# Performance work log

Hardware: AMD Instinct MI355X
Metric: run time of the kernel (lower is better)

Reference implementation:

```python
import jax, jax.numpy as jnp
import numpy as np

B, S, D_MODEL, H, D_K, D_V = 2, 2048, 1024, 16, 64, 64


def setup_inputs() -> dict:
    key = jax.random.key(0)
    ks = jax.random.split(key, 12)
    s = 0.02
    inp = {
        "Q": jax.random.normal(ks[0], (B, S, D_MODEL), jnp.float32),
        "K": jax.random.normal(ks[1], (B, S, D_MODEL), jnp.float32),
        "V": jax.random.normal(ks[2], (B, S, D_MODEL), jnp.float32),
        # causal 0/1 mask, broadcastable to [B, H, S, S]
        "mask": jnp.tril(jnp.ones((S, S), jnp.int32))[None, None, :, :],
        "Wq": jax.random.normal(ks[3], (D_MODEL, H * D_K), jnp.float32) * s,
        "bq": jnp.zeros((H * D_K,), jnp.float32),
        "Wk": jax.random.normal(ks[4], (D_MODEL, H * D_K), jnp.float32) * s,
        "bk": jnp.zeros((H * D_K,), jnp.float32),
        "Wv": jax.random.normal(ks[5], (D_MODEL, H * D_V), jnp.float32) * s,
        "bv": jnp.zeros((H * D_V,), jnp.float32),
        "Wo": jax.random.normal(ks[6], (H * D_V, D_MODEL), jnp.float32) * s,
        "bo": jnp.zeros((D_MODEL,), jnp.float32),
    }
    return inp


def reference(Q, K, V, mask, Wq, bq, Wk, bk, Wv, bv, Wo, bo):
    b = Q.shape[0]
    # project and split heads: [B, S, H*dk] -> [B, H, S, dk]
    q = (Q @ Wq + bq).reshape(b, -1, H, D_K).transpose(0, 2, 1, 3)
    k = (K @ Wk + bk).reshape(b, -1, H, D_K).transpose(0, 2, 1, 3)
    v = (V @ Wv + bv).reshape(b, -1, H, D_V).transpose(0, 2, 1, 3)
    scale = 1.0 / np.sqrt(D_K).astype(np.float32)
    scores = jnp.einsum("bhqd,bhkd->bhqk", q, k) * scale
    scores = jnp.where(mask == 0, jnp.float32(-1e9), scores)
    attn = jax.nn.softmax(scores, axis=-1)
    context = jnp.einsum("bhqk,bhkd->bhqd", attn, v)
    context = context.transpose(0, 2, 1, 3).reshape(b, -1, H * D_V)
    output = context @ Wo + bo  # dropout is identity in eval
    return output, attn
```

## Files before the change

### kernel.cpp

```cpp
#include <hip/hip_runtime.h>
#include <math.h>

#define S_LEN 2048
#define DMODEL 1024
#define NHEAD 16
#define HD 64
#define NBATCH 2

using short8  = __attribute__((ext_vector_type(8))) short;
using ushort8 = __attribute__((ext_vector_type(8))) unsigned short;
using floatx4 = __attribute__((ext_vector_type(4))) float;

__device__ __forceinline__ unsigned short f2b(float f) {
    unsigned int u = __float_as_uint(f);
    unsigned int r = (u + 0x7FFFu + ((u >> 16) & 1u)) >> 16;
    return (unsigned short)r;
}
__device__ __forceinline__ float b2f(unsigned short b) {
    return __uint_as_float(((unsigned int)b) << 16);
}

__device__ __forceinline__ void gll16(const void* g, void* l) {
    __builtin_amdgcn_global_load_lds(
        (const __attribute__((address_space(1))) unsigned int*)g,
        (__attribute__((address_space(3))) unsigned int*)l, 16, 0, 0);
}

__global__ __launch_bounds__(256)
void convert_bf16(const float* __restrict__ S0, const float* __restrict__ S1,
                  const float* __restrict__ S2,
                  unsigned short* __restrict__ D0, unsigned short* __restrict__ D1,
                  unsigned short* __restrict__ D2, int n4)
{
    const float* src = (blockIdx.z == 0) ? S0 : (blockIdx.z == 1) ? S1 : S2;
    unsigned short* dst = (blockIdx.z == 0) ? D0 : (blockIdx.z == 1) ? D1 : D2;
    int i = blockIdx.x * 256 + threadIdx.x;
    if (i < n4) {
        float4 v = ((const float4*)src)[i];
        ushort4 o;
        o.x = f2b(v.x); o.y = f2b(v.y); o.z = f2b(v.z); o.w = f2b(v.w);
        ((ushort4*)dst)[i] = o;
    }
}

__global__ __launch_bounds__(256)
void transpose_w(const float* __restrict__ W0, const float* __restrict__ W1,
                 const float* __restrict__ W2, const float* __restrict__ W3,
                 unsigned short* __restrict__ T0, unsigned short* __restrict__ T1,
                 unsigned short* __restrict__ T2, unsigned short* __restrict__ T3)
{
    __shared__ float t[64][65];
    const float* W; unsigned short* T;
    switch (blockIdx.z) {
        case 0: W = W0; T = T0; break;
        case 1: W = W1; T = T1; break;
        case 2: W = W2; T = T2; break;
        default: W = W3; T = T3; break;
    }
    const int tid = threadIdx.x;
    const int c0 = blockIdx.x * 64;
    const int r0 = blockIdx.y * 64;
    #pragma unroll
    for (int i = 0; i < 4; ++i) {
        int c = tid + i * 256;
        int r = c >> 4, off = (c & 15) * 4;
        float4 v = *(const float4*)(W + (size_t)(r0 + r) * DMODEL + c0 + off);
        t[r][off + 0] = v.x; t[r][off + 1] = v.y;
        t[r][off + 2] = v.z; t[r][off + 3] = v.w;
    }
    __syncthreads();
    #pragma unroll
    for (int i = 0; i < 4; ++i) {
        int c = tid + i * 256;
        int n = c >> 4, off = (c & 15) * 4;
        ushort4 o;
        o.x = f2b(t[off + 0][n]); o.y = f2b(t[off + 1][n]);
        o.z = f2b(t[off + 2][n]); o.w = f2b(t[off + 3][n]);
        *(ushort4*)(T + (size_t)(c0 + n) * DMODEL + r0 + off) = o;
    }
}

__global__ __launch_bounds__(256)
void gemm_qkv(const unsigned short* __restrict__ X0, const unsigned short* __restrict__ X1,
              const unsigned short* __restrict__ X2,
              const unsigned short* __restrict__ W0, const unsigned short* __restrict__ W1,
              const unsigned short* __restrict__ W2,
              const float* __restrict__ b0, const float* __restrict__ b1,
              const float* __restrict__ b2,
              unsigned short* __restrict__ o0, unsigned short* __restrict__ o1,
              unsigned short* __restrict__ o2)
{
    __shared__ unsigned short Xs[128 * 64];
    __shared__ unsigned short Ws[128 * 64];

    const unsigned short* X  = (blockIdx.z == 0) ? X0 : (blockIdx.z == 1) ? X1 : X2;
    const unsigned short* Wt = (blockIdx.z == 0) ? W0 : (blockIdx.z == 1) ? W1 : W2;
    const float* bias        = (blockIdx.z == 0) ? b0 : (blockIdx.z == 1) ? b1 : b2;
    unsigned short* outp     = (blockIdx.z == 0) ? o0 : (blockIdx.z == 1) ? o1 : o2;

    const int tid = threadIdx.x;
    const int lane = tid & 63, w = tid >> 6;
    const int l15 = lane & 15, l4 = lane >> 4;
    const int wr = w >> 1, wc = w & 1;
    const int row0 = blockIdx.y * 128;
    const int col0 = blockIdx.x * 128;

    const int srow = lane >> 3;
    const int sblk = (lane & 7) ^ srow;

    floatx4 acc[4][4] = {};

    for (int k0 = 0; k0 < DMODEL; k0 += 64) {
        __syncthreads();
        #pragma unroll
        for (int i = 0; i < 4; ++i)
            gll16(X + (size_t)(row0 + w * 32 + i * 8 + srow) * DMODEL + k0 + sblk * 8,
                  &Xs[(w * 32 + i * 8) * 64]);
        #pragma unroll
        for (int i = 0; i < 4; ++i)
            gll16(Wt + (size_t)(col0 + w * 32 + i * 8 + srow) * DMODEL + k0 + sblk * 8,
                  &Ws[(w * 32 + i * 8) * 64]);
        asm volatile("s_waitcnt vmcnt(0)" ::: "memory");
        __syncthreads();

        #pragma unroll
        for (int ks = 0; ks < 2; ++ks) {
            short8 a[4], b[4];
            #pragma unroll
            for (int m = 0; m < 4; ++m) {
                const int r = wr * 64 + m * 16 + l15;
                a[m] = *(const short8*)&Xs[r * 64 + (((ks * 4 + l4) ^ (r & 7)) << 3)];
            }
            #pragma unroll
            for (int n = 0; n < 4; ++n) {
                const int r = wc * 64 + n * 16 + l15;
                b[n] = *(const short8*)&Ws[r * 64 + (((ks * 4 + l4) ^ (r & 7)) << 3)];
            }
            #pragma unroll
            for (int m = 0; m < 4; ++m)
                #pragma unroll
                for (int n = 0; n < 4; ++n)
                    acc[m][n] = __builtin_amdgcn_mfma_f32_16x16x32_bf16(
                        a[m], b[n], acc[m][n], 0, 0, 0);
        }
    }

    float bl[4];
    #pragma unroll
    for (int n = 0; n < 4; ++n)
        bl[n] = bias[col0 + wc * 64 + n * 16 + l15];

    if (blockIdx.z != 2) {
        #pragma unroll
        for (int m = 0; m < 4; ++m)
            #pragma unroll
            for (int n = 0; n < 4; ++n) {
                const int gc = col0 + wc * 64 + n * 16 + l15;
                const int h = gc >> 6, d = gc & 63;
                #pragma unroll
                for (int reg = 0; reg < 4; ++reg) {
                    const int gr = row0 + wr * 64 + m * 16 + l4 * 4 + reg;
                    const int bb = gr >> 11, s = gr & 2047;
                    outp[(((size_t)bb * NHEAD + h) * S_LEN + s) * HD + d] =
                        f2b(acc[m][n][reg] + bl[n]);
                }
            }
    } else {
        #pragma unroll
        for (int m = 0; m < 4; ++m)
            #pragma unroll
            for (int n = 0; n < 4; ++n) {
                const int gc = col0 + wc * 64 + n * 16 + l15;
                const int h = gc >> 6, d = gc & 63;
                const int s0 = row0 + wr * 64 + m * 16 + l4 * 4;
                const int bb = s0 >> 11, sr = s0 & 2047;
                ushort4 pk;
                pk.x = f2b(acc[m][n][0] + bl[n]);
                pk.y = f2b(acc[m][n][1] + bl[n]);
                pk.z = f2b(acc[m][n][2] + bl[n]);
                pk.w = f2b(acc[m][n][3] + bl[n]);
                *(ushort4*)(outp + (((size_t)bb * NHEAD + h) * HD + d) * S_LEN + sr) = pk;
            }
    }
}

__global__ __launch_bounds__(256)
void gemm_out(const unsigned short* __restrict__ X, const unsigned short* __restrict__ Wt,
              const float* __restrict__ bias, float* __restrict__ out)
{
    __shared__ unsigned short Xs[128 * 64];
    __shared__ unsigned short Ws[64 * 64];

    const int tid = threadIdx.x;
    const int lane = tid & 63, w = tid >> 6;
    const int l15 = lane & 15, l4 = lane >> 4;
    const int wr = w >> 1, wc = w & 1;
    const int row0 = blockIdx.y * 128;
    const int col0 = blockIdx.x * 64;

    const int srow = lane >> 3;
    const int sblk = (lane & 7) ^ srow;

    floatx4 acc[4][2] = {};

    for (int k0 = 0; k0 < DMODEL; k0 += 64) {
        __syncthreads();
        #pragma unroll
        for (int i = 0; i < 4; ++i)
            gll16(X + (size_t)(row0 + w * 32 + i * 8 + srow) * DMODEL + k0 + sblk * 8,
                  &Xs[(w * 32 + i * 8) * 64]);
        #pragma unroll
        for (int i = 0; i < 2; ++i)
            gll16(Wt + (size_t)(col0 + w * 16 + i * 8 + srow) * DMODEL + k0 + sblk * 8,
                  &Ws[(w * 16 + i * 8) * 64]);
        asm volatile("s_waitcnt vmcnt(0)" ::: "memory");
        __syncthreads();

        #pragma unroll
        for (int ks = 0; ks < 2; ++ks) {
            short8 a[4], b[2];
            #pragma unroll
            for (int m = 0; m < 4; ++m) {
                const int r = wr * 64 + m * 16 + l15;
                a[m] = *(const short8*)&Xs[r * 64 + (((ks * 4 + l4) ^ (r & 7)) << 3)];
            }
            #pragma unroll
            for (int n = 0; n < 2; ++n) {
                const int r = wc * 32 + n * 16 + l15;
                b[n] = *(const short8*)&Ws[r * 64 + (((ks * 4 + l4) ^ (r & 7)) << 3)];
            }
            #pragma unroll
            for (int m = 0; m < 4; ++m)
                #pragma unroll
                for (int n = 0; n < 2; ++n)
                    acc[m][n] = __builtin_amdgcn_mfma_f32_16x16x32_bf16(
                        a[m], b[n], acc[m][n], 0, 0, 0);
        }
    }

    float bl[2];
    #pragma unroll
    for (int n = 0; n < 2; ++n)
        bl[n] = bias[col0 + wc * 32 + n * 16 + l15];

    #pragma unroll
    for (int m = 0; m < 4; ++m)
        #pragma unroll
        for (int n = 0; n < 2; ++n) {
            const int gc = col0 + wc * 32 + n * 16 + l15;
            #pragma unroll
            for (int reg = 0; reg < 4; ++reg) {
                const int gr = row0 + wr * 64 + m * 16 + l4 * 4 + reg;
                out[(size_t)gr * DMODEL + gc] = acc[m][n][reg] + bl[n];
            }
        }
}

__global__ __launch_bounds__(256)
void attn_mfma(const unsigned short* __restrict__ qg, const unsigned short* __restrict__ kg,
               const unsigned short* __restrict__ vtg, float* __restrict__ attn,
               unsigned short* __restrict__ ctx)
{
    __shared__ unsigned short Ks[2 * 64 * 64];
    __shared__ unsigned short Vt[64 * 64];
    __shared__ unsigned short Ps[64 * 88];

    const int tid = threadIdx.x;
    const int lane = tid & 63, w = tid >> 6;
    const int l15 = lane & 15, l4 = lane >> 4;

    const int i0 = blockIdx.x;
    const int local = i0 >> 3;
    const int bh = (i0 & 7) * 4 + (local & 3);
    const int qx = local >> 2;
    const int qb = (bh & 1) ? (31 - qx) : qx;
    const int row0 = qb * 64;

    const int srow = lane >> 3;
    const int sblk = (lane & 7) ^ srow;

    const float C2 = 0.18033688011112042f;

    const unsigned short* qh = qg + (size_t)bh * S_LEN * HD;
    const unsigned short* kh = kg + (size_t)bh * S_LEN * HD;
    const unsigned short* vth = vtg + (size_t)bh * HD * S_LEN;
    float* attnh = attn + (size_t)bh * S_LEN * S_LEN;

    short8 qa[2];
    #pragma unroll
    for (int ks = 0; ks < 2; ++ks)
        qa[ks] = *(const short8*)(qh + (size_t)(row0 + w * 16 + l15) * HD + ks * 32 + l4 * 8);

    const int nt = qb + 1;

    #pragma unroll
    for (int i = 0; i < 2; ++i)
        gll16(kh + (size_t)(w * 16 + i * 8 + srow) * HD + sblk * 8,
              &Ks[(w * 16 + i * 8) * 64]);

    float lsum[4] = {};
    for (int jt = 0; jt < nt; ++jt) {
        const int cur = jt & 1;
        __syncthreads();
        if (jt + 1 < nt) {
            #pragma unroll
            for (int i = 0; i < 2; ++i)
                gll16(kh + (size_t)((jt + 1) * 64 + w * 16 + i * 8 + srow) * HD + sblk * 8,
                      &Ks[(cur ^ 1) * 4096 + (w * 16 + i * 8) * 64]);
            asm volatile("s_waitcnt vmcnt(2)" ::: "memory");
        } else {
            asm volatile("s_waitcnt vmcnt(0)" ::: "memory");
        }
        __syncthreads();

        floatx4 sf[4] = {};
        #pragma unroll
        for (int ks = 0; ks < 2; ++ks) {
            short8 kb[4];
            #pragma unroll
            for (int c = 0; c < 4; ++c) {
                const int r = c * 16 + l15;
                kb[c] = *(const short8*)&Ks[cur * 4096 + r * 64
                                            + (((ks * 4 + l4) ^ (r & 7)) << 3)];
            }
            #pragma unroll
            for (int c = 0; c < 4; ++c)
                sf[c] = __builtin_amdgcn_mfma_f32_16x16x32_bf16(qa[ks], kb[c], sf[c], 0, 0, 0);
        }

        const int rbase = row0 + w * 16;
        if (jt * 64 + 63 <= rbase) {
            #pragma unroll
            for (int c = 0; c < 4; ++c)
                #pragma unroll
                for (int reg = 0; reg < 4; ++reg)
                    lsum[reg] += exp2f(sf[c][reg] * C2);
        } else {
            #pragma unroll
            for (int c = 0; c < 4; ++c) {
                const int jcol = jt * 64 + c * 16 + l15;
                #pragma unroll
                for (int reg = 0; reg < 4; ++reg) {
                    const int grow = rbase + l4 * 4 + reg;
                    lsum[reg] += (jcol <= grow) ? exp2f(sf[c][reg] * C2) : 0.f;
                }
            }
        }
    }

    float nl2[4];
    #pragma unroll
    for (int reg = 0; reg < 4; ++reg) {
        float s = lsum[reg];
        #pragma unroll
        for (int off = 1; off < 16; off <<= 1)
            s += __shfl_xor(s, off);
        nl2[reg] = -__log2f(s);
    }

    floatx4 o[4] = {};

    __syncthreads();
    #pragma unroll
    for (int i = 0; i < 2; ++i)
        gll16(kh + (size_t)(w * 16 + i * 8 + srow) * HD + sblk * 8,
              &Ks[(w * 16 + i * 8) * 64]);

    for (int jt = 0; jt < nt; ++jt) {
        const int buf = jt & 1;
        asm volatile("s_waitcnt vmcnt(0)" ::: "memory");
        __syncthreads();

        #pragma unroll
        for (int i = 0; i < 2; ++i)
            gll16(vth + (size_t)(w * 16 + i * 8 + srow) * S_LEN + jt * 64 + sblk * 8,
                  &Vt[(w * 16 + i * 8) * 64]);
        if (jt + 1 < nt) {
            #pragma unroll
            for (int i = 0; i < 2; ++i)
                gll16(kh + (size_t)((jt + 1) * 64 + w * 16 + i * 8 + srow) * HD + sblk * 8,
                      &Ks[(buf ^ 1) * 4096 + (w * 16 + i * 8) * 64]);
        }

        floatx4 sf[4] = {};
        #pragma unroll
        for (int ks = 0; ks < 2; ++ks) {
            short8 kb[4];
            #pragma unroll
            for (int c = 0; c < 4; ++c) {
                const int r = c * 16 + l15;
                kb[c] = *(const short8*)&Ks[buf * 4096 + r * 64
                                            + (((ks * 4 + l4) ^ (r & 7)) << 3)];
            }
            #pragma unroll
            for (int c = 0; c < 4; ++c)
                sf[c] = __builtin_amdgcn_mfma_f32_16x16x32_bf16(qa[ks], kb[c], sf[c], 0, 0, 0);
        }

        const int rbase = row0 + w * 16;
        const bool full = (jt * 64 + 63 <= rbase);
        #pragma unroll
        for (int c = 0; c < 4; ++c) {
            const int jcol = jt * 64 + c * 16 + l15;
            #pragma unroll
            for (int reg = 0; reg < 4; ++reg) {
                const int rl = w * 16 + l4 * 4 + reg;
                float p = exp2f(fmaf(sf[c][reg], C2, nl2[reg]));
                if (!full && jcol > rbase + l4 * 4 + reg) p = 0.f;
                Ps[rl * 88 + c * 16 + l15] = f2b(p);
            }
        }
        if (jt + 1 < nt) {
            asm volatile("s_waitcnt vmcnt(2)" ::: "memory");
        } else {
            asm volatile("s_waitcnt vmcnt(0)" ::: "memory");
        }
        __syncthreads();

        #pragma unroll
        for (int i2 = 0; i2 < 4; ++i2) {
            const int idx = tid + i2 * 256;
            const int r = idx >> 4, c4 = (idx & 15) * 4;
            const ushort4 pb = *(const ushort4*)&Ps[r * 88 + c4];
            floatx4 pf;
            pf[0] = b2f(pb.x); pf[1] = b2f(pb.y); pf[2] = b2f(pb.z); pf[3] = b2f(pb.w);
            __builtin_nontemporal_store(
                pf, (floatx4*)(attnh + (size_t)(row0 + r) * S_LEN + jt * 64 + c4));
        }

        #pragma unroll
        for (int ks = 0; ks < 2; ++ks) {
            const short8 pa = *(const short8*)&Ps[(w * 16 + l15) * 88 + ks * 32 + l4 * 8];
            #pragma unroll
            for (int c = 0; c < 4; ++c) {
                const int r = c * 16 + l15;
                const short8 vb = *(const short8*)&Vt[r * 64
                                                     + (((ks * 4 + l4) ^ (r & 7)) << 3)];
                o[c] = __builtin_amdgcn_mfma_f32_16x16x32_bf16(pa, vb, o[c], 0, 0, 0);
            }
        }
    }

    const int b = bh >> 4, h = bh & 15;
    #pragma unroll
    for (int c = 0; c < 4; ++c)
        #pragma unroll
        for (int reg = 0; reg < 4; ++reg) {
            const int gr = row0 + w * 16 + l4 * 4 + reg;
            const int d = c * 16 + l15;
            ctx[((size_t)b * S_LEN + gr) * DMODEL + h * HD + d] = f2b(o[c][reg]);
        }

    const floatx4 z4 = {0.f, 0.f, 0.f, 0.f};
    for (int jt = nt; jt < S_LEN / 64; ++jt) {
        #pragma unroll
        for (int i = 0; i < 4; ++i) {
            const int idx = tid + i * 256;
            const int r = idx >> 4, off = (idx & 15) * 4;
            __builtin_nontemporal_store(
                z4, (floatx4*)(attnh + (size_t)(row0 + r) * S_LEN + jt * 64 + off));
        }
    }
}

extern "C" void kernel_launch(void* const* d_in, const int* in_sizes, int n_in,
                              void* d_out, int out_size, void* d_ws, size_t ws_size,
                              hipStream_t stream)
{
    const float* Q  = (const float*)d_in[0];
    const float* K  = (const float*)d_in[1];
    const float* V  = (const float*)d_in[2];
    const float* Wq = (const float*)d_in[4];
    const float* bq = (const float*)d_in[5];
    const float* Wk = (const float*)d_in[6];
    const float* bk = (const float*)d_in[7];
    const float* Wv = (const float*)d_in[8];
    const float* bv = (const float*)d_in[9];
    const float* Wo = (const float*)d_in[10];
    const float* bo = (const float*)d_in[11];

    float* out  = (float*)d_out;
    float* attn = out + (size_t)NBATCH * S_LEN * DMODEL;

    const size_t per = (size_t)NBATCH * S_LEN * DMODEL;
    const size_t wsz = (size_t)DMODEL * DMODEL;
    unsigned short* Xq  = (unsigned short*)d_ws;
    unsigned short* Xk  = Xq + per;
    unsigned short* Xv  = Xk + per;
    unsigned short* Wtq = Xv + per;
    unsigned short* Wtk = Wtq + wsz;
    unsigned short* Wtv = Wtk + wsz;
    unsigned short* Wto = Wtv + wsz;
    unsigned short* qhw = Wto + wsz;
    unsigned short* khw = qhw + per;
    unsigned short* vhw = khw + per;
    unsigned short* ctx = vhw + per;

    const int n4 = (int)(per / 4);
    convert_bf16<<<dim3((n4 + 255) / 256, 1, 3), 256, 0, stream>>>(
        Q, K, V, Xq, Xk, Xv, n4);
    transpose_w<<<dim3(16, 16, 4), 256, 0, stream>>>(Wq, Wk, Wv, Wo, Wtq, Wtk, Wtv, Wto);

    gemm_qkv<<<dim3(DMODEL / 128, (NBATCH * S_LEN) / 128, 3), 256, 0, stream>>>(
        Xq, Xk, Xv, Wtq, Wtk, Wtv, bq, bk, bv, qhw, khw, vhw);

    attn_mfma<<<1024, 256, 0, stream>>>(qhw, khw, vhw, attn, ctx);

    gemm_out<<<dim3(DMODEL / 64, (NBATCH * S_LEN) / 128), 256, 0, stream>>>(
        ctx, Wto, bo, out);
}
```

Before: 231.3 us.

## Split attention into separate row-stats kernel with larger query tiles

Moves the softmax denominator pass out of the fused attention kernel into a separate kernel that handles 128 query rows per block, so each K tile loaded into shared memory feeds twice as many MFMAs. The normalizers go to a global workspace and the write kernel reads them instead of recomputing them. This aims to cut K reloads and give the stats pass more arithmetic per load. It costs an extra launch, a small global round trip, and half as many blocks in the stats pass.

```diff
diff --git a/kernel.cpp b/kernel.cpp
--- a/kernel.cpp
+++ b/kernel.cpp
@@ -257,9 +257,119 @@
 }
 
 __global__ __launch_bounds__(256)
-void attn_mfma(const unsigned short* __restrict__ qg, const unsigned short* __restrict__ kg,
-               const unsigned short* __restrict__ vtg, float* __restrict__ attn,
-               unsigned short* __restrict__ ctx)
+void attn_stats(const unsigned short* __restrict__ qg, const unsigned short* __restrict__ kg,
+                float* __restrict__ nl2g)
+{
+    __shared__ unsigned short Ks[2 * 64 * 64];
+
+    const int tid = threadIdx.x;
+    const int lane = tid & 63, w = tid >> 6;
+    const int l15 = lane & 15, l4 = lane >> 4;
+
+    const int i0 = blockIdx.x;
+    const int local = i0 >> 3;
+    const int bh = (i0 & 7) * 4 + (local & 3);
+    const int qx = local >> 2;
+    const int qb = (bh & 1) ? (15 - qx) : qx;
+    const int row0 = qb * 128;
+
+    const int srow = lane >> 3;
+    const int sblk = (lane & 7) ^ srow;
+
+    const float C2 = 0.18033688011112042f;
+
+    const unsigned short* qh = qg + (size_t)bh * S_LEN * HD;
+    const unsigned short* kh = kg + (size_t)bh * S_LEN * HD;
+
+    short8 qa[2][2];
+    #pragma unroll
+    for (int m = 0; m < 2; ++m)
+        #pragma unroll
+        for (int ks = 0; ks < 2; ++ks)
+            qa[m][ks] = *(const short8*)(qh + (size_t)(row0 + w * 32 + m * 16 + l15) * HD
+                                         + ks * 32 + l4 * 8);
+
+    const int nt = 2 * qb + 2;
+
+    #pragma unroll
+    for (int i = 0; i < 2; ++i)
+        gll16(kh + (size_t)(w * 16 + i * 8 + srow) * HD + sblk * 8,
+              &Ks[(w * 16 + i * 8) * 64]);
+
+    float lsum[2][4] = {};
+    for (int jt = 0; jt < nt; ++jt) {
+        const int cur = jt & 1;
+        __syncthreads();
+        if (jt + 1 < nt) {
+            #pragma unroll
+            for (int i = 0; i < 2; ++i)
+                gll16(kh + (size_t)((jt + 1) * 64 + w * 16 + i * 8 + srow) * HD + sblk * 8,
+                      &Ks[(cur ^ 1) * 4096 + (w * 16 + i * 8) * 64]);
+            asm volatile("s_waitcnt vmcnt(2)" ::: "memory");
+        } else {
+            asm volatile("s_waitcnt vmcnt(0)" ::: "memory");
+        }
+        __syncthreads();
+
+        floatx4 sf[2][4] = {};
+        #pragma unroll
+        for (int ks = 0; ks < 2; ++ks) {
+            short8 kb[4];
+            #pragma unroll
+            for (int c = 0; c < 4; ++c) {
+                const int r = c * 16 + l15;
+                kb[c] = *(const short8*)&Ks[cur * 4096 + r * 64
+                                            + (((ks * 4 + l4) ^ (r & 7)) << 3)];
+            }
+            #pragma unroll
+            for (int m = 0; m < 2; ++m)
+                #pragma unroll
+                for (int c = 0; c < 4; ++c)
+                    sf[m][c] = __builtin_amdgcn_mfma_f32_16x16x32_bf16(
+                        qa[m][ks], kb[c], sf[m][c], 0, 0, 0);
+        }
+
+        #pragma unroll
+        for (int m = 0; m < 2; ++m) {
+            const int rbase = row0 + w * 32 + m * 16;
+            if (jt * 64 + 63 <= rbase) {
+                #pragma unroll
+                for (int c = 0; c < 4; ++c)
+                    #pragma unroll
+                    for (int reg = 0; reg < 4; ++reg)
+                        lsum[m][reg] += exp2f(sf[m][c][reg] * C2);
+            } else {
+                #pragma unroll
+                for (int c = 0; c < 4; ++c) {
+                    const int jcol = jt * 64 + c * 16 + l15;
+                    #pragma unroll
+                    for (int reg = 0; reg < 4; ++reg) {
+                        const int grow = rbase + l4 * 4 + reg;
+                        lsum[m][reg] += (jcol <= grow) ? exp2f(sf[m][c][reg] * C2) : 0.f;
+                    }
+                }
+            }
+        }
+    }
+
+    #pragma unroll
+    for (int m = 0; m < 2; ++m)
+        #pragma unroll
+        for (int reg = 0; reg < 4; ++reg) {
+            float s = lsum[m][reg];
+            #pragma unroll
+            for (int off = 1; off < 16; off <<= 1)
+                s += __shfl_xor(s, off);
+            if (l15 == 0)
+                nl2g[(size_t)bh * S_LEN + row0 + w * 32 + m * 16 + l4 * 4 + reg] =
+                    -__log2f(s);
+        }
+}
+
+__global__ __launch_bounds__(256)
+void attn_write(const unsigned short* __restrict__ qg, const unsigned short* __restrict__ kg,
+                const unsigned short* __restrict__ vtg, const float* __restrict__ nl2g,
+                float* __restrict__ attn, unsigned short* __restrict__ ctx)
 {
     __shared__ unsigned short Ks[2 * 64 * 64];
     __shared__ unsigned short Vt[64 * 64];
@@ -291,6 +401,12 @@
     for (int ks = 0; ks < 2; ++ks)
         qa[ks] = *(const short8*)(qh + (size_t)(row0 + w * 16 + l15) * HD + ks * 32 + l4 * 8);
 
+    float nl2[4];
+    {
+        const float4 nv = *(const float4*)(nl2g + (size_t)bh * S_LEN + row0 + w * 16 + l4 * 4);
+        nl2[0] = nv.x; nl2[1] = nv.y; nl2[2] = nv.z; nl2[3] = nv.w;
+    }
+
     const int nt = qb + 1;
 
     #pragma unroll
@@ -298,74 +414,7 @@
         gll16(kh + (size_t)(w * 16 + i * 8 + srow) * HD + sblk * 8,
               &Ks[(w * 16 + i * 8) * 64]);
 
-    float lsum[4] = {};
-    for (int jt = 0; jt < nt; ++jt) {
-        const int cur = jt & 1;
-        __syncthreads();
-        if (jt + 1 < nt) {
-            #pragma unroll
-            for (int i = 0; i < 2; ++i)
-                gll16(kh + (size_t)((jt + 1) * 64 + w * 16 + i * 8 + srow) * HD + sblk * 8,
-                      &Ks[(cur ^ 1) * 4096 + (w * 16 + i * 8) * 64]);
-            asm volatile("s_waitcnt vmcnt(2)" ::: "memory");
-        } else {
-            asm volatile("s_waitcnt vmcnt(0)" ::: "memory");
-        }
-        __syncthreads();
-
-        floatx4 sf[4] = {};
-        #pragma unroll
-        for (int ks = 0; ks < 2; ++ks) {
-            short8 kb[4];
-            #pragma unroll
-            for (int c = 0; c < 4; ++c) {
-                const int r = c * 16 + l15;
-                kb[c] = *(const short8*)&Ks[cur * 4096 + r * 64
-                                            + (((ks * 4 + l4) ^ (r & 7)) << 3)];
-            }
-            #pragma unroll
-            for (int c = 0; c < 4; ++c)
-                sf[c] = __builtin_amdgcn_mfma_f32_16x16x32_bf16(qa[ks], kb[c], sf[c], 0, 0, 0);
-        }
-
-        const int rbase = row0 + w * 16;
-        if (jt * 64 + 63 <= rbase) {
-            #pragma unroll
-            for (int c = 0; c < 4; ++c)
-                #pragma unroll
-                for (int reg = 0; reg < 4; ++reg)
-                    lsum[reg] += exp2f(sf[c][reg] * C2);
-        } else {
-            #pragma unroll
-            for (int c = 0; c < 4; ++c) {
-                const int jcol = jt * 64 + c * 16 + l15;
-                #pragma unroll
-                for (int reg = 0; reg < 4; ++reg) {
-                    const int grow = rbase + l4 * 4 + reg;
-                    lsum[reg] += (jcol <= grow) ? exp2f(sf[c][reg] * C2) : 0.f;
-                }
-            }
-        }
-    }
-
-    float nl2[4];
-    #pragma unroll
-    for (int reg = 0; reg < 4; ++reg) {
-        float s = lsum[reg];
-        #pragma unroll
-        for (int off = 1; off < 16; off <<= 1)
-            s += __shfl_xor(s, off);
-        nl2[reg] = -__log2f(s);
-    }
-
     floatx4 o[4] = {};
-
-    __syncthreads();
-    #pragma unroll
-    for (int i = 0; i < 2; ++i)
-        gll16(kh + (size_t)(w * 16 + i * 8 + srow) * HD + sblk * 8,
-              &Ks[(w * 16 + i * 8) * 64]);
-
     for (int jt = 0; jt < nt; ++jt) {
         const int buf = jt & 1;
         asm volatile("s_waitcnt vmcnt(0)" ::: "memory");
@@ -495,6 +544,7 @@
     unsigned short* khw = qhw + per;
     unsigned short* vhw = khw + per;
     unsigned short* ctx = vhw + per;
+    float* nl2g = (float*)(ctx + per);
 
     const int n4 = (int)(per / 4);
     convert_bf16<<<dim3((n4 + 255) / 256, 1, 3), 256, 0, stream>>>(
@@ -504,7 +554,8 @@
     gemm_qkv<<<dim3(DMODEL / 128, (NBATCH * S_LEN) / 128, 3), 256, 0, stream>>>(
         Xq, Xk, Xv, Wtq, Wtk, Wtv, bq, bk, bv, qhw, khw, vhw);
 
-    attn_mfma<<<1024, 256, 0, stream>>>(qhw, khw, vhw, attn, ctx);
+    attn_stats<<<512, 256, 0, stream>>>(qhw, khw, nl2g);
+    attn_write<<<1024, 256, 0, stream>>>(qhw, khw, vhw, nl2g, attn, ctx);
 
     gemm_out<<<dim3(DMODEL / 64, (NBATCH * S_LEN) / 128), 256, 0, stream>>>(
         ctx, Wto, bo, out);
```

After: 258.1 us. 11.6% more time.
